# Performance work log

Measured on AMD Instinct MI355X. Metric: run time of the kernel, lower is better.

## Reference

```python
import jax, jax.numpy as jnp
import numpy as np

B, N, S, V, D, H, DEPTH, C = 4, 60000, 1024, 8, 256, 4, 4, 20
DH = D // H
MH = 4 * D
SCALE = 1.0 / float(np.sqrt(DH))


def _ln(x, g, b):
    m = x.mean(-1, keepdims=True)
    v = ((x - m) ** 2).mean(-1, keepdims=True)
    return g * (x - m) * jax.lax.rsqrt(v + 1e-5) + b


def _mha(q_in, kv_in, q_w, q_b, kv_w, kv_b, p_w, p_b):
    Bq, Tq, _ = q_in.shape
    Tk = kv_in.shape[1]
    q = (q_in @ q_w + q_b).reshape(Bq, Tq, H, DH)
    kv = (kv_in @ kv_w + kv_b).reshape(Bq, Tk, 2, H, DH)
    k, v = kv[:, :, 0], kv[:, :, 1]
    a = jax.nn.softmax(jnp.einsum('bqhd,bkhd->bhqk', q, k) * SCALE, axis=-1)
    o = jnp.einsum('bhqk,bkhd->bqhd', a, v).reshape(Bq, Tq, D)
    return o @ p_w + p_b, a


def _encoder(x, qkv_w, qkv_b, p_w, p_b, ln1_g, ln1_b, ln2_g, ln2_b, m_w1, m_b1, m_w2, m_b2):
    attns = []
    for d in range(DEPTH):
        h = _ln(x, ln1_g[d], ln1_b[d])
        o, a = _mha(h, h, qkv_w[d][:, :D], qkv_b[d][:D], qkv_w[d][:, D:], qkv_b[d][D:], p_w[d], p_b[d])
        x = x + o
        h = _ln(x, ln2_g[d], ln2_b[d])
        x = x + jax.nn.gelu(h @ m_w1[d] + m_b1[d]) @ m_w2[d] + m_b2[d]
        attns.append(a)
    return x, attns


def _seg_mean(x, ids):
    # scatter-mean (avg_grouping): x [N,F], ids [N] -> [S,F]; empty segments -> 0 (nan-fix in source)
    s = jax.ops.segment_sum(x, ids, num_segments=S)
    cnt = jax.ops.segment_sum(jnp.ones((x.shape[0],), x.dtype), ids, num_segments=S)
    return jnp.where(cnt[:, None] > 0, s / jnp.maximum(cnt, 1.0)[:, None], 0.0)


def _forward(supervoxel, point_feat, point_coord, image_view_tokens, cls_token, cls_pos_emb, view_pos_emb,
             pos_w1, pos_b1, pos_w2, pos_b2, pos_w3, pos_b3,
             enc_qkv_w, enc_qkv_b, enc_proj_w, enc_proj_b, enc_ln1_g, enc_ln1_b, enc_ln2_g, enc_ln2_b,
             enc_mlp_w1, enc_mlp_b1, enc_mlp_w2, enc_mlp_b2,
             dec_q_w, dec_q_b, dec_kv_w, dec_kv_b, dec_proj_w, dec_proj_b,
             dec_lnq_g, dec_lnq_b, dec_lnkv_g, dec_lnkv_b, dec_ln2_g, dec_ln2_b,
             dec_mlp_w1, dec_mlp_b1, dec_mlp_w2, dec_mlp_b2,
             head2d_w, head2d_b, head3d_w, head3d_b):
    # ---- view (2D) branch: [cls; view tokens] + pos, encoder idx 0 ----
    view_tok = jnp.concatenate([jnp.broadcast_to(cls_token, (B, C, D)), image_view_tokens], axis=1)
    view_pos = jnp.concatenate([jnp.broadcast_to(cls_pos_emb, (B, C, D)),
                                jnp.broadcast_to(view_pos_emb, (B, V, D))], axis=1)
    attn_view, _ = _encoder(view_tok + view_pos, enc_qkv_w[0], enc_qkv_b[0], enc_proj_w[0], enc_proj_b[0],
                            enc_ln1_g[0], enc_ln1_b[0], enc_ln2_g[0], enc_ln2_b[0],
                            enc_mlp_w1[0], enc_mlp_b1[0], enc_mlp_w2[0], enc_mlp_b2[0])
    mct_logits_2d = attn_view[:, :C].mean(-1)
    # ---- supervoxel scatter-mean pooling (the ragged core), vectorized over batch ----
    pooled_feat = jax.vmap(_seg_mean)(point_feat, supervoxel)      # [B,S,D]
    pooled_coord = jax.vmap(_seg_mean)(point_coord, supervoxel)    # [B,S,3]
    mean_target = jnp.take_along_axis(pooled_feat, supervoxel[..., None], axis=1)  # gather back [B,N,D]
    consistent_loss = jnp.mean((point_feat - mean_target) ** 2)
    # ---- coord positional MLP (3 layers) ----
    h = jax.nn.relu(pooled_coord @ pos_w1 + pos_b1)
    h = jax.nn.relu(h @ pos_w2 + pos_b2)
    pos = h @ pos_w3 + pos_b3
    # ---- voxel (3D) branch: [cls; pooled supervoxel tokens], encoder idx 1 ----
    vox_tok = jnp.concatenate([jnp.broadcast_to(cls_token, (B, C, D)), pooled_feat], axis=1)
    vox_pos = jnp.concatenate([jnp.broadcast_to(cls_pos_emb, (B, C, D)), pos], axis=1)
    vox_enc, _ = _encoder(vox_tok + vox_pos, enc_qkv_w[1], enc_qkv_b[1], enc_proj_w[1], enc_proj_b[1],
                          enc_ln1_g[1], enc_ln1_b[1], enc_ln2_g[1], enc_ln2_b[1],
                          enc_mlp_w1[1], enc_mlp_b1[1], enc_mlp_w2[1], enc_mlp_b2[1])
    mct_logits_3d = vox_enc[:, :C].mean(-1)
    # ---- interlance decoder: dual cross-attention, stream 0 = view->voxel, 1 = voxel->view ----
    view_x, vox_x = attn_view, vox_enc
    sim_losses = []
    for d in range(DEPTH):
        vq = _ln(view_x, dec_lnq_g[0, d], dec_lnq_b[0, d])
        xk = _ln(vox_x, dec_lnkv_g[0, d], dec_lnkv_b[0, d])
        xq = _ln(vox_x, dec_lnq_g[1, d], dec_lnq_b[1, d])
        vk = _ln(view_x, dec_lnkv_g[1, d], dec_lnkv_b[1, d])
        v_out, a = _mha(vq, xk, dec_q_w[0, d], dec_q_b[0, d], dec_kv_w[0, d], dec_kv_b[0, d], dec_proj_w[0, d], dec_proj_b[0, d])
        x_out, _ = _mha(xq, vk, dec_q_w[1, d], dec_q_b[1, d], dec_kv_w[1, d], dec_kv_b[1, d], dec_proj_w[1, d], dec_proj_b[1, d])
        view_x = view_x + v_out
        vox_x = vox_x + x_out
        hv = _ln(view_x, dec_ln2_g[0, d], dec_ln2_b[0, d])
        view_x = view_x + jax.nn.gelu(hv @ dec_mlp_w1[0, d] + dec_mlp_b1[0, d]) @ dec_mlp_w2[0, d] + dec_mlp_b2[0, d]
        hx = _ln(vox_x, dec_ln2_g[1, d], dec_ln2_b[1, d])
        vox_x = vox_x + jax.nn.gelu(hx @ dec_mlp_w1[1, d] + dec_mlp_b1[1, d]) @ dec_mlp_w2[1, d] + dec_mlp_b2[1, d]
        # pairwise token-sim loss on cls-cls block of head-averaged cross-attention
        sim = a.mean(1)[:, :C, :C]  # [B,C,C]
        lv = -jnp.diagonal(jax.nn.log_softmax(sim, axis=-1), axis1=1, axis2=2).mean(-1)
        lx = -jnp.diagonal(jax.nn.log_softmax(jnp.swapaxes(sim, 1, 2), axis=-1), axis1=1, axis2=2).mean(-1)
        sim_losses.append((lv + lx) * 0.5)
    token_sim_loss = jnp.stack(sim_losses).mean()
    cross_cls = (vox_x[:, :C] + view_x[:, :C]) * 0.5
    cross_mct_logits = cross_cls.mean(-1)
    # ---- CAM heads (cam_on_attn=True, pool='avg') ----
    voxel_cam = jax.nn.relu(vox_enc[:, C:]) @ head3d_w + head3d_b    # [B,S,C]
    view_cam = image_view_tokens @ head2d_w + head2d_b               # [B,V,C]
    cam_logits_3d = voxel_cam.mean(1)
    cam_logits_2d = view_cam.mean(1)
    return (cross_mct_logits, mct_logits_2d, mct_logits_3d, cam_logits_2d, cam_logits_3d,
            consistent_loss, token_sim_loss, voxel_cam)


def setup_inputs():
    key = jax.random.key(0)
    ks = iter(jax.random.split(key, 64))
    nrm = lambda *sh: jax.random.normal(next(ks), sh, jnp.float32)
    w = lambda *sh: 0.02 * jax.random.normal(next(ks), sh, jnp.float32)
    inp = dict(
        point_feat=nrm(B, N, D),
        point_coord=jax.random.uniform(next(ks), (B, N, 3), jnp.float32) * 100.0,
        image_view_tokens=nrm(B, V, D),
        supervoxel=jax.random.randint(next(ks), (B, N), 0, S),
        cls_token=w(1, C, D), cls_pos_emb=w(1, C, D), view_pos_emb=w(1, V, D),
        pos_w1=w(3, D), pos_b1=jnp.zeros((D,)), pos_w2=w(D, D), pos_b2=jnp.zeros((D,)),
        pos_w3=w(D, D), pos_b3=jnp.zeros((D,)),
        enc_qkv_w=w(2, DEPTH, D, 3 * D), enc_qkv_b=jnp.zeros((2, DEPTH, 3 * D)),
        enc_proj_w=w(2, DEPTH, D, D), enc_proj_b=jnp.zeros((2, DEPTH, D)),
        enc_ln1_g=jnp.ones((2, DEPTH, D)), enc_ln1_b=jnp.zeros((2, DEPTH, D)),
        enc_ln2_g=jnp.ones((2, DEPTH, D)), enc_ln2_b=jnp.zeros((2, DEPTH, D)),
        enc_mlp_w1=w(2, DEPTH, D, MH), enc_mlp_b1=jnp.zeros((2, DEPTH, MH)),
        enc_mlp_w2=w(2, DEPTH, MH, D), enc_mlp_b2=jnp.zeros((2, DEPTH, D)),
        dec_q_w=w(2, DEPTH, D, D), dec_q_b=jnp.zeros((2, DEPTH, D)),
        dec_kv_w=w(2, DEPTH, D, 2 * D), dec_kv_b=jnp.zeros((2, DEPTH, 2 * D)),
        dec_proj_w=w(2, DEPTH, D, D), dec_proj_b=jnp.zeros((2, DEPTH, D)),
        dec_lnq_g=jnp.ones((2, DEPTH, D)), dec_lnq_b=jnp.zeros((2, DEPTH, D)),
        dec_lnkv_g=jnp.ones((2, DEPTH, D)), dec_lnkv_b=jnp.zeros((2, DEPTH, D)),
        dec_ln2_g=jnp.ones((2, DEPTH, D)), dec_ln2_b=jnp.zeros((2, DEPTH, D)),
        dec_mlp_w1=w(2, DEPTH, D, MH), dec_mlp_b1=jnp.zeros((2, DEPTH, MH)),
        dec_mlp_w2=w(2, DEPTH, MH, D), dec_mlp_b2=jnp.zeros((2, DEPTH, D)),
        head2d_w=w(D, C), head2d_b=jnp.zeros((C,)),
        head3d_w=w(D, C), head3d_b=jnp.zeros((C,)),
    )
    return inp


def reference(point_feat, point_coord, image_view_tokens, supervoxel, cls_token, cls_pos_emb, view_pos_emb,
              pos_w1, pos_b1, pos_w2, pos_b2, pos_w3, pos_b3,
              enc_qkv_w, enc_qkv_b, enc_proj_w, enc_proj_b, enc_ln1_g, enc_ln1_b, enc_ln2_g, enc_ln2_b,
              enc_mlp_w1, enc_mlp_b1, enc_mlp_w2, enc_mlp_b2,
              dec_q_w, dec_q_b, dec_kv_w, dec_kv_b, dec_proj_w, dec_proj_b,
              dec_lnq_g, dec_lnq_b, dec_lnkv_g, dec_lnkv_b, dec_ln2_g, dec_ln2_b,
              dec_mlp_w1, dec_mlp_b1, dec_mlp_w2, dec_mlp_b2,
              head2d_w, head2d_b, head3d_w, head3d_b):
    return _forward(supervoxel, point_feat, point_coord, image_view_tokens, cls_token, cls_pos_emb, view_pos_emb,
                    pos_w1, pos_b1, pos_w2, pos_b2, pos_w3, pos_b3,
                    enc_qkv_w, enc_qkv_b, enc_proj_w, enc_proj_b, enc_ln1_g, enc_ln1_b, enc_ln2_g, enc_ln2_b,
                    enc_mlp_w1, enc_mlp_b1, enc_mlp_w2, enc_mlp_b2,
                    dec_q_w, dec_q_b, dec_kv_w, dec_kv_b, dec_proj_w, dec_proj_b,
                    dec_lnq_g, dec_lnq_b, dec_lnkv_g, dec_lnkv_b, dec_ln2_g, dec_ln2_b,
                    dec_mlp_w1, dec_mlp_b1, dec_mlp_w2, dec_mlp_b2,
                    head2d_w, head2d_b, head3d_w, head3d_b)
```

## Files before the change

### kernel.cpp

```cpp
#include <hip/hip_runtime.h>

namespace {

constexpr int kB = 4, kN = 60000, kS = 1024, kV = 8, kD = 256, kH = 4, kDepth = 4, kC = 20;
constexpr int kDH = 64;
constexpr int kMH = 1024;
constexpr int kTV = kC + kV;
constexpr int kTX = kC + kS;
constexpr float kScale = 0.125f;

constexpr int NSLICE = 8;
constexpr int DC = 16;
constexpr int DCH = kD / DC;

template <int BM, int BN, int TM, int TN, int ACT, bool TRB, bool PRELU>
__global__ __launch_bounds__(256) void gemm_k(
    const float* __restrict__ A, const float* __restrict__ Bm,
    const float* __restrict__ bias, const float* __restrict__ Res,
    float* __restrict__ C, int M, int N, int K, int lda, int ldb, int ldc,
    long sAb, long sAh, long sBb, long sBh, long sCb, long sCh, int Hdim, float alpha)
{
  constexpr int KT = 16;
  constexpr int MB = TM / 4;
  constexpr int NB = TN / 4;
  constexpr int AE = BM * KT / 256;
  constexpr int BE = BN * KT / 256;
  __shared__ float As[KT][BM + 4];
  __shared__ float Bs[KT][BN + 4];
  const int z = blockIdx.z;
  const int bi = z / Hdim, hi = z - bi * Hdim;
  A += (long)bi * sAb + (long)hi * sAh;
  Bm += (long)bi * sBb + (long)hi * sBh;
  C += (long)bi * sCb + (long)hi * sCh;
  const float* R = Res;
  if (R) R += (long)bi * sCb + (long)hi * sCh;
  const int n0 = blockIdx.x * BN, m0 = blockIdx.y * BM;
  const int tid = threadIdx.x;
  const int tx = tid % 16, ty = tid / 16;
  float acc[TM][TN];
#pragma unroll
  for (int i = 0; i < TM; i++)
#pragma unroll
    for (int j = 0; j < TN; j++) acc[i][j] = 0.f;

  float ra[AE], rb[BE];
#pragma unroll
  for (int i = 0; i < AE; i++) {
    int e = tid + i * 256;
    int row = e >> 4, kk = e & 15;
    int gm = m0 + row, gk = kk;
    float v = 0.f;
    if (gm < M && gk < K) v = A[(long)gm * lda + gk];
    if (PRELU) v = fmaxf(v, 0.f);
    ra[i] = v;
  }
#pragma unroll
  for (int i = 0; i < BE; i++) {
    int e = tid + i * 256;
    int kk, col;
    if (TRB) { kk = e & 15; col = e >> 4; }
    else     { col = e % BN; kk = e / BN; }
    int gk = kk, gn = n0 + col;
    float v = 0.f;
    if (gk < K && gn < N) v = TRB ? Bm[(long)gn * ldb + gk] : Bm[(long)gk * ldb + gn];
    rb[i] = v;
  }

  for (int k0 = 0; k0 < K; k0 += KT) {
#pragma unroll
    for (int i = 0; i < AE; i++) {
      int e = tid + i * 256;
      As[e & 15][e >> 4] = ra[i];
    }
#pragma unroll
    for (int i = 0; i < BE; i++) {
      int e = tid + i * 256;
      int kk, col;
      if (TRB) { kk = e & 15; col = e >> 4; }
      else     { col = e % BN; kk = e / BN; }
      Bs[kk][col] = rb[i];
    }
    __syncthreads();
    if (k0 + KT < K) {
      const int kn = k0 + KT;
#pragma unroll
      for (int i = 0; i < AE; i++) {
        int e = tid + i * 256;
        int row = e >> 4, kk = e & 15;
        int gm = m0 + row, gk = kn + kk;
        float v = 0.f;
        if (gm < M && gk < K) v = A[(long)gm * lda + gk];
        if (PRELU) v = fmaxf(v, 0.f);
        ra[i] = v;
      }
#pragma unroll
      for (int i = 0; i < BE; i++) {
        int e = tid + i * 256;
        int kk, col;
        if (TRB) { kk = e & 15; col = e >> 4; }
        else     { col = e % BN; kk = e / BN; }
        int gk = kn + kk, gn = n0 + col;
        float v = 0.f;
        if (gk < K && gn < N) v = TRB ? Bm[(long)gn * ldb + gk] : Bm[(long)gk * ldb + gn];
        rb[i] = v;
      }
    }
#pragma unroll
    for (int kk = 0; kk < KT; kk++) {
      const float4* Ar = reinterpret_cast<const float4*>(&As[kk][0]);
      const float4* Br = reinterpret_cast<const float4*>(&Bs[kk][0]);
      float4 af[MB], bf[NB];
#pragma unroll
      for (int ib = 0; ib < MB; ib++) af[ib] = Ar[ty + ib * 16];
#pragma unroll
      for (int jb = 0; jb < NB; jb++) bf[jb] = Br[tx + jb * 16];
      float av[TM], bv[TN];
#pragma unroll
      for (int ib = 0; ib < MB; ib++) {
        av[ib * 4 + 0] = af[ib].x; av[ib * 4 + 1] = af[ib].y;
        av[ib * 4 + 2] = af[ib].z; av[ib * 4 + 3] = af[ib].w;
      }
#pragma unroll
      for (int jb = 0; jb < NB; jb++) {
        bv[jb * 4 + 0] = bf[jb].x; bv[jb * 4 + 1] = bf[jb].y;
        bv[jb * 4 + 2] = bf[jb].z; bv[jb * 4 + 3] = bf[jb].w;
      }
#pragma unroll
      for (int i = 0; i < TM; i++)
#pragma unroll
        for (int j = 0; j < TN; j++) acc[i][j] += av[i] * bv[j];
    }
    __syncthreads();
  }
#pragma unroll
  for (int i = 0; i < TM; i++) {
    int gm = m0 + (i >> 2) * 64 + ty * 4 + (i & 3);
    if (gm >= M) continue;
#pragma unroll
    for (int j = 0; j < TN; j++) {
      int gn = n0 + (j >> 2) * 64 + tx * 4 + (j & 3);
      if (gn >= N) continue;
      float v = acc[i][j] * alpha;
      if (bias) v += bias[gn];
      if (ACT == 1) v = fmaxf(v, 0.f);
      else if (ACT == 2) {
        float u = v;
        float t = 0.7978845608028654f * (u + 0.044715f * u * u * u);
        v = u / (1.f + __expf(-2.f * t));
      }
      if (R) v += R[(long)gm * ldc + gn];
      C[(long)gm * ldc + gn] = v;
    }
  }
}

__global__ __launch_bounds__(256) void ln_k(const float* __restrict__ x,
                                            const float* __restrict__ g,
                                            const float* __restrict__ b,
                                            float* __restrict__ o, int rows)
{
  __shared__ float red[256];
  __shared__ float stat;
  int row = blockIdx.x;
  int t = threadIdx.x;
  float v = x[(long)row * kD + t];
  red[t] = v;
  __syncthreads();
  for (int s = 128; s > 0; s >>= 1) { if (t < s) red[t] += red[t + s]; __syncthreads(); }
  if (t == 0) stat = red[0] * (1.f / kD);
  __syncthreads();
  float m = stat;
  float d = v - m;
  red[t] = d * d;
  __syncthreads();
  for (int s = 128; s > 0; s >>= 1) { if (t < s) red[t] += red[t + s]; __syncthreads(); }
  if (t == 0) stat = rsqrtf(red[0] * (1.f / kD) + 1e-5f);
  __syncthreads();
  o[(long)row * kD + t] = g[t] * d * stat + b[t];
}

__global__ __launch_bounds__(256) void softmax_k(float* __restrict__ s, int L)
{
  long row = blockIdx.x;
  float* p = s + row * (long)L;
  int t = threadIdx.x;
  float rv[8];
  int nc = (L + 255) >> 8;
  float mx = -1e30f;
  for (int c = 0; c < nc; c++) {
    int i = t + c * 256;
    rv[c] = (i < L) ? p[i] : -1e30f;
    mx = fmaxf(mx, rv[c]);
  }
  __shared__ float red[256];
  __shared__ float bb;
  red[t] = mx; __syncthreads();
  for (int st = 128; st > 0; st >>= 1) { if (t < st) red[t] = fmaxf(red[t], red[t + st]); __syncthreads(); }
  if (t == 0) bb = red[0];
  __syncthreads();
  float bm = bb;
  float sum = 0.f;
  for (int c = 0; c < nc; c++) {
    int i = t + c * 256;
    if (i < L) { rv[c] = __expf(rv[c] - bm); sum += rv[c]; }
  }
  red[t] = sum; __syncthreads();
  for (int st = 128; st > 0; st >>= 1) { if (t < st) red[t] += red[t + st]; __syncthreads(); }
  if (t == 0) bb = 1.f / red[0];
  __syncthreads();
  float inv = bb;
  for (int c = 0; c < nc; c++) {
    int i = t + c * 256;
    if (i < L) p[i] = rv[c] * inv;
  }
}

__global__ __launch_bounds__(256) void segsum_k(const float* __restrict__ pf,
                                                const int* __restrict__ sv,
                                                float* __restrict__ part)
{
  __shared__ float acc[kS * DC];
  int t = threadIdx.x;
  for (int i = t; i < kS * DC; i += 256) acc[i] = 0.f;
  __syncthreads();
  int dc = blockIdx.x, sl = blockIdx.y, b = blockIdx.z;
  const int per = kN / NSLICE;
  int n0 = sl * per, n1 = n0 + per;
  int ld_ = t & (DC - 1), pg = t >> 4;
  for (int base = n0 + pg; base < n1; base += 16 * 8) {
    int s[8]; float v[8];
#pragma unroll
    for (int u = 0; u < 8; u++) {
      int n = base + u * 16;
      bool ok = n < n1;
      s[u] = ok ? sv[b * kN + n] : -1;
      v[u] = ok ? pf[((long)b * kN + n) * kD + dc * DC + ld_] : 0.f;
    }
#pragma unroll
    for (int u = 0; u < 8; u++)
      if (s[u] >= 0) atomicAdd(&acc[s[u] * DC + ld_], v[u]);
  }
  __syncthreads();
  float* outp = part + (((long)(b * NSLICE + sl) * DCH + dc) * (kS * DC));
  for (int i = t; i < kS * DC; i += 256) outp[i] = acc[i];
}

__global__ __launch_bounds__(256) void segmeta_k(const float* __restrict__ pc,
                                                 const int* __restrict__ sv,
                                                 float* __restrict__ cpart,
                                                 float* __restrict__ csumpart)
{
  __shared__ float meta[kS * 4];
  int t = threadIdx.x;
  for (int i = t; i < kS * 4; i += 256) meta[i] = 0.f;
  __syncthreads();
  int sl = blockIdx.x, b = blockIdx.y;
  const int per = kN / NSLICE;
  int n0 = sl * per, n1 = n0 + per;
  for (int base = n0 + t; base < n1; base += 256 * 4) {
    int s[4]; float cx[4], cy[4], cz[4];
#pragma unroll
    for (int u = 0; u < 4; u++) {
      int n = base + u * 256;
      bool ok = n < n1;
      s[u] = ok ? sv[b * kN + n] : -1;
      long p = ((long)b * kN + n) * 3;
      cx[u] = ok ? pc[p + 0] : 0.f;
      cy[u] = ok ? pc[p + 1] : 0.f;
      cz[u] = ok ? pc[p + 2] : 0.f;
    }
#pragma unroll
    for (int u = 0; u < 4; u++)
      if (s[u] >= 0) {
        atomicAdd(&meta[s[u] * 4 + 0], 1.f);
        atomicAdd(&meta[s[u] * 4 + 1], cx[u]);
        atomicAdd(&meta[s[u] * 4 + 2], cy[u]);
        atomicAdd(&meta[s[u] * 4 + 3], cz[u]);
      }
  }
  __syncthreads();
  float* oc = cpart + (long)(b * NSLICE + sl) * kS;
  for (int i = t; i < kS; i += 256) oc[i] = meta[i * 4];
  float* os = csumpart + (long)(b * NSLICE + sl) * kS * 3;
  for (int i = t; i < kS * 3; i += 256) {
    int s2 = i / 3, j = i - s2 * 3;
    os[i] = meta[s2 * 4 + 1 + j];
  }
}

__global__ void cntfin_k(const float* __restrict__ cpart, float* __restrict__ counts)
{
  int i = blockIdx.x * 256 + threadIdx.x;
  if (i >= kB * kS) return;
  int b = i / kS, s = i - b * kS;
  float c = 0.f;
  for (int sl = 0; sl < NSLICE; sl++) c += cpart[(long)(b * NSLICE + sl) * kS + s];
  counts[i] = c;
}

__global__ void poolfin_k(const float* __restrict__ part, const float* __restrict__ counts,
                          float* __restrict__ pooled)
{
  long i = (long)blockIdx.x * 256 + threadIdx.x;
  if (i >= (long)kB * kS * kD) return;
  int d = (int)(i % kD);
  long bs = i / kD;
  int s = (int)(bs % kS), b = (int)(bs / kS);
  int dc = d / DC, dl = d - dc * DC;
  float sum = 0.f;
  for (int sl = 0; sl < NSLICE; sl++)
    sum += part[(((long)(b * NSLICE + sl) * DCH + dc) * (kS * DC)) + s * DC + dl];
  float c = counts[b * kS + s];
  pooled[i] = (c > 0.5f) ? sum / c : 0.f;
}

__global__ void coordfin_k(const float* __restrict__ csumpart, const float* __restrict__ counts,
                           float* __restrict__ pcoord)
{
  int i = blockIdx.x * 256 + threadIdx.x;
  if (i >= kB * kS * 3) return;
  int bs = i / 3, j = i - bs * 3;
  int b = bs / kS, s = bs - b * kS;
  float sum = 0.f;
  for (int sl = 0; sl < NSLICE; sl++)
    sum += csumpart[((long)(b * NSLICE + sl) * kS + s) * 3 + j];
  float c = counts[bs];
  pcoord[i] = (c > 0.5f) ? sum / c : 0.f;
}

__global__ __launch_bounds__(256) void closs_k(const float* __restrict__ pf,
                                               const int* __restrict__ sv,
                                               const float* __restrict__ pooled,
                                               float* __restrict__ outp)
{
  const long total = (long)kB * kN * (kD / 4);
  float a = 0.f;
  for (long i = (long)blockIdx.x * 256 + threadIdx.x; i < total; i += (long)gridDim.x * 256) {
    long pnt = i >> 6;
    int dc = (int)(i & 63);
    int b = (int)(pnt / kN);
    int s = sv[pnt];
    float4 v = ((const float4*)pf)[i];
    float4 m = ((const float4*)pooled)[((long)b * kS + s) * (kD / 4) + dc];
    float dx = v.x - m.x, dy = v.y - m.y, dz = v.z - m.z, dw = v.w - m.w;
    a += dx * dx + dy * dy + dz * dz + dw * dw;
  }
  __shared__ float red[256];
  red[threadIdx.x] = a; __syncthreads();
  for (int s = 128; s > 0; s >>= 1) { if (threadIdx.x < s) red[threadIdx.x] += red[threadIdx.x + s]; __syncthreads(); }
  if (threadIdx.x == 0) atomicAdd(outp, red[0]);
}

__global__ void build_k(const float* __restrict__ cls, const float* __restrict__ clspos,
                        const float* __restrict__ tok, const float* __restrict__ pos,
                        float* __restrict__ x, int T, int Tt, int posBatched)
{
  long i = (long)blockIdx.x * 256 + threadIdx.x;
  long tot = (long)kB * T * kD;
  if (i >= tot) return;
  int d = (int)(i % kD);
  long bt = i / kD;
  int t = (int)(bt % T), b = (int)(bt / T);
  float v;
  if (t < kC) v = cls[t * kD + d] + clspos[t * kD + d];
  else {
    int tt = t - kC;
    v = tok[((long)b * Tt + tt) * kD + d] +
        pos[((long)(posBatched ? b * Tt : 0) + tt) * kD + d];
  }
  x[i] = v;
}

__global__ __launch_bounds__(64) void simloss_k(const float* __restrict__ probs,
                                                float* __restrict__ accum)
{
  int b = blockIdx.x;
  __shared__ float sim[kC][kC];
  int t = threadIdx.x;
  for (int e = t; e < kC * kC; e += 64) {
    int i = e / kC, j = e - i * kC;
    float s = 0.f;
    for (int h = 0; h < kH; h++)
      s += probs[(((long)(b * kH + h)) * kTV + i) * kTX + j];
    sim[i][j] = s * (1.f / kH);
  }
  __syncthreads();
  float local = 0.f;
  if (t < kC) {
    int i = t;
    float mx = -1e30f;
    for (int j = 0; j < kC; j++) mx = fmaxf(mx, sim[i][j]);
    float se = 0.f;
    for (int j = 0; j < kC; j++) se += expf(sim[i][j] - mx);
    float dr = sim[i][i] - mx - logf(se);
    float mc = -1e30f;
    for (int j = 0; j < kC; j++) mc = fmaxf(mc, sim[j][i]);
    float sc = 0.f;
    for (int j = 0; j < kC; j++) sc += expf(sim[j][i] - mc);
    float dcl = sim[i][i] - mc - logf(sc);
    local = dr + dcl;
  }
  for (int o = 32; o > 0; o >>= 1) local += __shfl_down(local, o);
  if (t == 0) atomicAdd(accum, local * (-0.5f / kC));
}

__global__ __launch_bounds__(64) void meanD_k(const float* __restrict__ x,
                                              float* __restrict__ o, int T)
{
  int bc = blockIdx.x;
  int b = bc / kC, c = bc - b * kC;
  const float* r = x + ((long)b * T + c) * kD;
  float s = 0.f;
  for (int d = threadIdx.x; d < kD; d += 64) s += r[d];
  for (int w = 32; w > 0; w >>= 1) s += __shfl_down(s, w);
  if (threadIdx.x == 0) o[bc] = s * (1.f / kD);
}

__global__ __launch_bounds__(64) void cross_k(const float* __restrict__ xv,
                                              const float* __restrict__ xw,
                                              float* __restrict__ o)
{
  int bc = blockIdx.x;
  int b = bc / kC, c = bc - b * kC;
  const float* rv = xv + ((long)b * kTX + c) * kD;
  const float* rw = xw + ((long)b * kTV + c) * kD;
  float s = 0.f;
  for (int d = threadIdx.x; d < kD; d += 64) s += 0.5f * (rv[d] + rw[d]);
  for (int w = 32; w > 0; w >>= 1) s += __shfl_down(s, w);
  if (threadIdx.x == 0) o[bc] = s * (1.f / kD);
}

__global__ __launch_bounds__(256) void cam3d_k(const float* __restrict__ vc,
                                               float* __restrict__ o)
{
  __shared__ float red[256];
  int bc = blockIdx.x;
  int b = bc / kC, c = bc - b * kC;
  float s = 0.f;
  for (int t = threadIdx.x; t < kS; t += 256) s += vc[((long)b * kS + t) * kC + c];
  red[threadIdx.x] = s; __syncthreads();
  for (int st = 128; st > 0; st >>= 1) { if (threadIdx.x < st) red[threadIdx.x] += red[threadIdx.x + st]; __syncthreads(); }
  if (threadIdx.x == 0) o[bc] = red[0] * (1.f / kS);
}

__global__ void meanv_k(const float* __restrict__ ivt, float* __restrict__ mv)
{
  int i = blockIdx.x * 256 + threadIdx.x;
  if (i >= kB * kD) return;
  int b = i / kD, d = i - b * kD;
  float s = 0.f;
  for (int v = 0; v < kV; v++) s += ivt[((long)b * kV + v) * kD + d];
  mv[i] = s * (1.f / kV);
}

__global__ __launch_bounds__(64) void cam2d_k(const float* __restrict__ mv,
                                              const float* __restrict__ w2,
                                              const float* __restrict__ b2,
                                              float* __restrict__ o)
{
  int bc = blockIdx.x;
  int b = bc / kC, c = bc - b * kC;
  float s = 0.f;
  for (int d = threadIdx.x; d < kD; d += 64) s += mv[b * kD + d] * w2[d * kC + c];
  for (int w = 32; w > 0; w >>= 1) s += __shfl_down(s, w);
  if (threadIdx.x == 0) o[bc] = s + b2[c];
}

__global__ void fin_k(const float* __restrict__ cl, const float* __restrict__ ts,
                      float* __restrict__ outp)
{
  outp[400] = cl[0] * (1.f / ((float)kB * (float)kN * (float)kD));
  outp[401] = ts[0] * (1.f / (kDepth * kB));
}

static void gemm_disp(hipStream_t st, const float* A, const float* Bm, const float* bias,
                      const float* Res, float* C, int M, int N, int K,
                      int lda, int ldb, int ldc,
                      long sAb, long sAh, long sBb, long sBh, long sCb, long sCh,
                      int Z, int Hdim, float alpha, int act, bool trb, bool prelu)
{
  dim3 blk(256, 1, 1);
  long bigBlocks = (long)((M + 127) / 128) * ((N + 127) / 128) * Z;
  bool big = (N >= 96) && (bigBlocks >= 384);
#define GARGS A, Bm, bias, Res, C, M, N, K, lda, ldb, ldc, sAb, sAh, sBb, sBh, sCb, sCh, Hdim, alpha
  if (big) {
    dim3 g((N + 127) / 128, (M + 127) / 128, Z);
    if (prelu)          gemm_k<128, 128, 8, 8, 0, false, true ><<<g, blk, 0, st>>>(GARGS);
    else if (trb)       gemm_k<128, 128, 8, 8, 0, true,  false><<<g, blk, 0, st>>>(GARGS);
    else if (act == 1)  gemm_k<128, 128, 8, 8, 1, false, false><<<g, blk, 0, st>>>(GARGS);
    else if (act == 2)  gemm_k<128, 128, 8, 8, 2, false, false><<<g, blk, 0, st>>>(GARGS);
    else                gemm_k<128, 128, 8, 8, 0, false, false><<<g, blk, 0, st>>>(GARGS);
  } else {
    dim3 g((N + 63) / 64, (M + 63) / 64, Z);
    if (prelu)          gemm_k<64, 64, 4, 4, 0, false, true ><<<g, blk, 0, st>>>(GARGS);
    else if (trb)       gemm_k<64, 64, 4, 4, 0, true,  false><<<g, blk, 0, st>>>(GARGS);
    else if (act == 1)  gemm_k<64, 64, 4, 4, 1, false, false><<<g, blk, 0, st>>>(GARGS);
    else if (act == 2)  gemm_k<64, 64, 4, 4, 2, false, false><<<g, blk, 0, st>>>(GARGS);
    else                gemm_k<64, 64, 4, 4, 0, false, false><<<g, blk, 0, st>>>(GARGS);
  }
#undef GARGS
}

static void linear(hipStream_t st, const float* A, const float* W, const float* bias,
                   const float* Res, float* C, int M, int N, int K, int act)
{
  gemm_disp(st, A, W, bias, Res, C, M, N, K, K, N, N, 0, 0, 0, 0, 0, 0, 1, 1, 1.f, act, false, false);
}

static void attention(hipStream_t st, const float* qb, int ldq, const float* kb,
                      const float* vb, int ldkv, int Tq, int Tk, float* P, float* O)
{
  gemm_disp(st, qb, kb, nullptr, nullptr, P, Tq, Tk, kDH, ldq, ldkv, Tk,
            (long)Tq * ldq, kDH, (long)Tk * ldkv, kDH, (long)kH * Tq * Tk, (long)Tq * Tk,
            kB * kH, kH, kScale, 0, true, false);
  softmax_k<<<dim3(kB * kH * Tq), dim3(256), 0, st>>>(P, Tk);
  gemm_disp(st, P, vb, nullptr, nullptr, O, Tq, kDH, Tk, Tk, ldkv, kD,
            (long)kH * Tq * Tk, (long)Tq * Tk, (long)Tk * ldkv, kDH, (long)Tq * kD, kDH,
            kB * kH, kH, 1.f, 0, false, false);
}

}

extern "C" void kernel_launch(void* const* d_in, const int* in_sizes, int n_in,
                              void* d_out, int out_size, void* d_ws, size_t ws_size,
                              hipStream_t stream)
{
  (void)in_sizes; (void)n_in; (void)out_size; (void)ws_size;
  const float* point_feat  = (const float*)d_in[0];
  const float* point_coord = (const float*)d_in[1];
  const float* ivt         = (const float*)d_in[2];
  const int*   sv          = (const int*)d_in[3];
  const float* cls_token   = (const float*)d_in[4];
  const float* cls_pos     = (const float*)d_in[5];
  const float* view_pos    = (const float*)d_in[6];
  const float* pos_w1 = (const float*)d_in[7];
  const float* pos_b1 = (const float*)d_in[8];
  const float* pos_w2 = (const float*)d_in[9];
  const float* pos_b2 = (const float*)d_in[10];
  const float* pos_w3 = (const float*)d_in[11];
  const float* pos_b3 = (const float*)d_in[12];
  const float* enc_qkv_w  = (const float*)d_in[13];
  const float* enc_qkv_b  = (const float*)d_in[14];
  const float* enc_proj_w = (const float*)d_in[15];
  const float* enc_proj_b = (const float*)d_in[16];
  const float* enc_ln1_g  = (const float*)d_in[17];
  const float* enc_ln1_b  = (const float*)d_in[18];
  const float* enc_ln2_g  = (const float*)d_in[19];
  const float* enc_ln2_b  = (const float*)d_in[20];
  const float* enc_mlp_w1 = (const float*)d_in[21];
  const float* enc_mlp_b1 = (const float*)d_in[22];
  const float* enc_mlp_w2 = (const float*)d_in[23];
  const float* enc_mlp_b2 = (const float*)d_in[24];
  const float* dec_q_w    = (const float*)d_in[25];
  const float* dec_q_b    = (const float*)d_in[26];
  const float* dec_kv_w   = (const float*)d_in[27];
  const float* dec_kv_b   = (const float*)d_in[28];
  const float* dec_proj_w = (const float*)d_in[29];
  const float* dec_proj_b = (const float*)d_in[30];
  const float* dec_lnq_g  = (const float*)d_in[31];
  const float* dec_lnq_b  = (const float*)d_in[32];
  const float* dec_lnkv_g = (const float*)d_in[33];
  const float* dec_lnkv_b = (const float*)d_in[34];
  const float* dec_ln2_g  = (const float*)d_in[35];
  const float* dec_ln2_b  = (const float*)d_in[36];
  const float* dec_mlp_w1 = (const float*)d_in[37];
  const float* dec_mlp_b1 = (const float*)d_in[38];
  const float* dec_mlp_w2 = (const float*)d_in[39];
  const float* dec_mlp_b2 = (const float*)d_in[40];
  const float* head2d_w = (const float*)d_in[41];
  const float* head2d_b = (const float*)d_in[42];
  const float* head3d_w = (const float*)d_in[43];
  const float* head3d_b = (const float*)d_in[44];
  float* out = (float*)d_out;

  float* w = (float*)d_ws;
  size_t off = 0;
  auto alloc = [&](size_t n) { float* p = w + off; off += n; return p; };

  const size_t scores_sz = (size_t)kB * kH * kTX * kTX;
  const size_t probs_sz  = (size_t)kB * kH * kTV * kTX;
  float* regionA  = alloc(scores_sz + 2 * probs_sz);
  float* seg_part = regionA;
  float* scores   = regionA;
  float* probs1   = regionA + scores_sz;
  float* probs2   = probs1 + probs_sz;

  float* cpart    = alloc((size_t)kB * NSLICE * kS);
  float* csumpart = alloc((size_t)kB * NSLICE * kS * 3);
  float* counts   = alloc((size_t)kB * kS);
  float* pooled   = alloc((size_t)kB * kS * kD);
  float* closs    = alloc(1);
  float* simacc   = alloc(1);
  float* pcoord   = alloc((size_t)kB * kS * 3);
  float* ph1      = alloc((size_t)kB * kS * kD);
  float* ph2      = alloc((size_t)kB * kS * kD);
  float* posb     = alloc((size_t)kB * kS * kD);
  float* x_view   = alloc((size_t)kB * kTV * kD);
  float* h_view   = alloc((size_t)kB * kTV * kD);
  float* qkv_view = alloc((size_t)kB * kTV * 3 * kD);
  float* o_view   = alloc((size_t)kB * kTV * kD);
  float* mlp_view = alloc((size_t)kB * kTV * kMH);
  float* x_vox    = alloc((size_t)kB * kTX * kD);
  float* h_vox    = alloc((size_t)kB * kTX * kD);
  float* qkv_vox  = alloc((size_t)kB * kTX * 3 * kD);
  float* o_vox    = alloc((size_t)kB * kTX * kD);
  float* mlp_vox  = alloc((size_t)kB * kTX * kMH);
  float* q_small  = alloc((size_t)kB * kTV * kD);
  float* kv_big   = alloc((size_t)kB * kTX * 2 * kD);
  float* q_big    = alloc((size_t)kB * kTX * kD);
  float* kv_small = alloc((size_t)kB * kTV * 2 * kD);
  float* meanv    = alloc((size_t)kB * kD);

  hipMemsetAsync(closs, 0, 2 * sizeof(float), stream);

  segsum_k<<<dim3(DCH, NSLICE, kB), 256, 0, stream>>>(point_feat, sv, seg_part);
  segmeta_k<<<dim3(NSLICE, kB), 256, 0, stream>>>(point_coord, sv, cpart, csumpart);
  cntfin_k<<<dim3((kB * kS + 255) / 256), 256, 0, stream>>>(cpart, counts);
  poolfin_k<<<dim3((kB * kS * kD + 255) / 256), 256, 0, stream>>>(seg_part, counts, pooled);
  coordfin_k<<<dim3((kB * kS * 3 + 255) / 256), 256, 0, stream>>>(csumpart, counts, pcoord);
  closs_k<<<dim3(2048), 256, 0, stream>>>(point_feat, sv, pooled, closs);

  linear(stream, pcoord, pos_w1, pos_b1, nullptr, ph1, kB * kS, kD, 3, 1);
  linear(stream, ph1, pos_w2, pos_b2, nullptr, ph2, kB * kS, kD, kD, 1);
  linear(stream, ph2, pos_w3, pos_b3, nullptr, posb, kB * kS, kD, kD, 0);

  build_k<<<dim3(((unsigned)(kB * kTV * kD) + 255) / 256), 256, 0, stream>>>(
      cls_token, cls_pos, ivt, view_pos, x_view, kTV, kV, 0);
  build_k<<<dim3(((unsigned)(kB * kTX * kD) + 255) / 256), 256, 0, stream>>>(
      cls_token, cls_pos, pooled, posb, x_vox, kTX, kS, 1);

  auto encoder = [&](float* x, int T, int e, float* h, float* qkv, float* o, float* mlp) {
    int M = kB * T;
    for (int dl = 0; dl < kDepth; dl++) {
      int wi = e * kDepth + dl;
      ln_k<<<dim3(M), 256, 0, stream>>>(x, enc_ln1_g + wi * kD, enc_ln1_b + wi * kD, h, M);
      linear(stream, h, enc_qkv_w + (long)wi * kD * 3 * kD, enc_qkv_b + (long)wi * 3 * kD,
             nullptr, qkv, M, 3 * kD, kD, 0);
      attention(stream, qkv, 3 * kD, qkv + kD, qkv + 2 * kD, 3 * kD, T, T, scores, o);
      linear(stream, o, enc_proj_w + (long)wi * kD * kD, enc_proj_b + (long)wi * kD, x, x, M, kD, kD, 0);
      ln_k<<<dim3(M), 256, 0, stream>>>(x, enc_ln2_g + wi * kD, enc_ln2_b + wi * kD, h, M);
      linear(stream, h, enc_mlp_w1 + (long)wi * kD * kMH, enc_mlp_b1 + (long)wi * kMH,
             nullptr, mlp, M, kMH, kD, 2);
      linear(stream, mlp, enc_mlp_w2 + (long)wi * kMH * kD, enc_mlp_b2 + (long)wi * kD, x, x, M, kD, kMH, 0);
    }
  };
  encoder(x_view, kTV, 0, h_view, qkv_view, o_view, mlp_view);
  meanD_k<<<dim3(kB * kC), 64, 0, stream>>>(x_view, out + 80, kTV);

  encoder(x_vox, kTX, 1, h_vox, qkv_vox, o_vox, mlp_vox);
  meanD_k<<<dim3(kB * kC), 64, 0, stream>>>(x_vox, out + 160, kTX);

  gemm_disp(stream, x_vox + (long)kC * kD, head3d_w, head3d_b, nullptr, out + 402,
            kS, kC, kD, kD, kC, kC,
            (long)kTX * kD, 0, 0, 0, (long)kS * kC, 0,
            kB, 1, 1.f, 0, false, true);
  cam3d_k<<<dim3(kB * kC), 256, 0, stream>>>(out + 402, out + 320);
  meanv_k<<<dim3((kB * kD + 255) / 256), 256, 0, stream>>>(ivt, meanv);
  cam2d_k<<<dim3(kB * kC), 64, 0, stream>>>(meanv, head2d_w, head2d_b, out + 240);

  for (int dl = 0; dl < kDepth; dl++) {
    int w0 = dl, w1 = kDepth + dl;
    ln_k<<<dim3(kB * kTV), 256, 0, stream>>>(x_view, dec_lnq_g + w0 * kD, dec_lnq_b + w0 * kD, h_view, kB * kTV);
    ln_k<<<dim3(kB * kTX), 256, 0, stream>>>(x_vox, dec_lnkv_g + w0 * kD, dec_lnkv_b + w0 * kD, h_vox, kB * kTX);
    linear(stream, h_view, dec_q_w + (long)w0 * kD * kD, dec_q_b + (long)w0 * kD, nullptr, q_small, kB * kTV, kD, kD, 0);
    linear(stream, h_vox, dec_kv_w + (long)w0 * kD * 2 * kD, dec_kv_b + (long)w0 * 2 * kD, nullptr, kv_big, kB * kTX, 2 * kD, kD, 0);
    attention(stream, q_small, kD, kv_big, kv_big + kD, 2 * kD, kTV, kTX, probs1, o_view);
    simloss_k<<<dim3(kB), 64, 0, stream>>>(probs1, simacc);

    ln_k<<<dim3(kB * kTX), 256, 0, stream>>>(x_vox, dec_lnq_g + w1 * kD, dec_lnq_b + w1 * kD, h_vox, kB * kTX);
    ln_k<<<dim3(kB * kTV), 256, 0, stream>>>(x_view, dec_lnkv_g + w1 * kD, dec_lnkv_b + w1 * kD, h_view, kB * kTV);
    linear(stream, h_vox, dec_q_w + (long)w1 * kD * kD, dec_q_b + (long)w1 * kD, nullptr, q_big, kB * kTX, kD, kD, 0);
    linear(stream, h_view, dec_kv_w + (long)w1 * kD * 2 * kD, dec_kv_b + (long)w1 * 2 * kD, nullptr, kv_small, kB * kTV, 2 * kD, kD, 0);
    attention(stream, q_big, kD, kv_small, kv_small + kD, 2 * kD, kTX, kTV, probs2, o_vox);

    linear(stream, o_view, dec_proj_w + (long)w0 * kD * kD, dec_proj_b + (long)w0 * kD, x_view, x_view, kB * kTV, kD, kD, 0);
    linear(stream, o_vox, dec_proj_w + (long)w1 * kD * kD, dec_proj_b + (long)w1 * kD, x_vox, x_vox, kB * kTX, kD, kD, 0);

    ln_k<<<dim3(kB * kTV), 256, 0, stream>>>(x_view, dec_ln2_g + w0 * kD, dec_ln2_b + w0 * kD, h_view, kB * kTV);
    linear(stream, h_view, dec_mlp_w1 + (long)w0 * kD * kMH, dec_mlp_b1 + (long)w0 * kMH, nullptr, mlp_view, kB * kTV, kMH, kD, 2);
    linear(stream, mlp_view, dec_mlp_w2 + (long)w0 * kMH * kD, dec_mlp_b2 + (long)w0 * kD, x_view, x_view, kB * kTV, kD, kMH, 0);
    ln_k<<<dim3(kB * kTX), 256, 0, stream>>>(x_vox, dec_ln2_g + w1 * kD, dec_ln2_b + w1 * kD, h_vox, kB * kTX);
    linear(stream, h_vox, dec_mlp_w1 + (long)w1 * kD * kMH, dec_mlp_b1 + (long)w1 * kMH, nullptr, mlp_vox, kB * kTX, kMH, kD, 2);
    linear(stream, mlp_vox, dec_mlp_w2 + (long)w1 * kMH * kD, dec_mlp_b2 + (long)w1 * kD, x_vox, x_vox, kB * kTX, kD, kMH, 0);
  }

  cross_k<<<dim3(kB * kC), 64, 0, stream>>>(x_vox, x_view, out + 0);
  fin_k<<<dim3(1), 1, 0, stream>>>(closs, simacc, out);
}
```

Before: 5.315 ms.

## Add split-bf16 MFMA GEMM for large voxel-branch matmuls and attention

Adds a matrix-core GEMM kernel that splits each fp32 operand into high and low bf16 parts and accumulates three MFMA products, approximating fp32 accuracy. It uses a swizzled LDS layout and register prefetch of the next K tile. The kernel replaces the scalar fp32 GEMM for the voxel encoder, decoder voxel-side linears and voxel attention. It also retunes the segment-sum kernel to 512 threads with a smaller unroll. The split adds conversion work and carries a small precision risk versus true fp32.

```diff
diff --git a/kernel.cpp b/kernel.cpp
--- a/kernel.cpp
+++ b/kernel.cpp
@@ -12,6 +12,184 @@
 constexpr int NSLICE = 8;
 constexpr int DC = 16;
 constexpr int DCH = kD / DC;
+
+typedef short bf16x8 __attribute__((ext_vector_type(8)));
+typedef float f32x4 __attribute__((ext_vector_type(4)));
+typedef int   int4v __attribute__((ext_vector_type(4)));
+
+__device__ inline short f2bf_rne(float f) {
+  unsigned u = __builtin_bit_cast(unsigned, f);
+  u += 0x7FFF + ((u >> 16) & 1);
+  return (short)(u >> 16);
+}
+__device__ inline float bf2f(short s) {
+  unsigned u = ((unsigned)(unsigned short)s) << 16;
+  return __builtin_bit_cast(float, u);
+}
+__device__ inline void split8(const float* v, int4v& hi, int4v& lo) {
+  short h[8], l[8];
+#pragma unroll
+  for (int j = 0; j < 8; j++) {
+    h[j] = f2bf_rne(v[j]);
+    l[j] = f2bf_rne(v[j] - bf2f(h[j]));
+  }
+#pragma unroll
+  for (int j = 0; j < 4; j++) {
+    hi[j] = (int)(unsigned short)h[2*j] | ((int)(unsigned short)h[2*j+1] << 16);
+    lo[j] = (int)(unsigned short)l[2*j] | ((int)(unsigned short)l[2*j+1] << 16);
+  }
+}
+
+template <int ACT, bool TRB>
+__global__ __launch_bounds__(256) void mgemm_k(
+    const float* __restrict__ A, const float* __restrict__ Bm,
+    const float* __restrict__ bias, const float* __restrict__ Res,
+    float* __restrict__ C, int M, int N, int K, int lda, int ldb, int ldc,
+    long sAb, long sAh, long sBb, long sBh, long sCb, long sCh, int Hdim, float alpha)
+{
+  __shared__ char lds[2 * 128 * 128];
+  char* Alds = lds;
+  char* Blds = lds + 128 * 128;
+  const int z = blockIdx.z;
+  const int bi = z / Hdim, hi_ = z - bi * Hdim;
+  A += (long)bi * sAb + (long)hi_ * sAh;
+  Bm += (long)bi * sBb + (long)hi_ * sBh;
+  C += (long)bi * sCb + (long)hi_ * sCh;
+  const float* R = Res;
+  if (R) R += (long)bi * sCb + (long)hi_ * sCh;
+  const int n0 = blockIdx.x * 128, m0 = blockIdx.y * 128;
+  const int tid = threadIdx.x;
+  const int lane = tid & 63, wid = tid >> 6;
+  const int wm = wid >> 1, wn = wid & 1;
+
+  f32x4 acc[4][4];
+#pragma unroll
+  for (int i = 0; i < 4; i++)
+#pragma unroll
+    for (int j = 0; j < 4; j++) { acc[i][j][0]=0.f; acc[i][j][1]=0.f; acc[i][j][2]=0.f; acc[i][j][3]=0.f; }
+
+  int4v paH[2], paL[2], pbH[2], pbL[2];
+
+  auto loadA = [&](int k0) {
+#pragma unroll
+    for (int i = 0; i < 2; i++) {
+      int c = tid + i * 256;
+      int row = c >> 2, kg = c & 3;
+      int gm = m0 + row;
+      int gk0 = k0 + kg * 8;
+      float v[8];
+      if (gm < M && gk0 + 8 <= K) {
+        float4 x = *(const float4*)(A + (long)gm * lda + gk0);
+        float4 y = *(const float4*)(A + (long)gm * lda + gk0 + 4);
+        v[0]=x.x; v[1]=x.y; v[2]=x.z; v[3]=x.w; v[4]=y.x; v[5]=y.y; v[6]=y.z; v[7]=y.w;
+      } else {
+#pragma unroll
+        for (int j = 0; j < 8; j++)
+          v[j] = (gm < M && gk0 + j < K) ? A[(long)gm * lda + gk0 + j] : 0.f;
+      }
+      split8(v, paH[i], paL[i]);
+    }
+  };
+  auto loadB = [&](int k0) {
+#pragma unroll
+    for (int i = 0; i < 2; i++) {
+      int c = tid + i * 256;
+      float v[8];
+      if (TRB) {
+        int row = c >> 2, kg = c & 3;
+        int gn = n0 + row, gk0 = k0 + kg * 8;
+        if (gn < N && gk0 + 8 <= K) {
+          float4 x = *(const float4*)(Bm + (long)gn * ldb + gk0);
+          float4 y = *(const float4*)(Bm + (long)gn * ldb + gk0 + 4);
+          v[0]=x.x; v[1]=x.y; v[2]=x.z; v[3]=x.w; v[4]=y.x; v[5]=y.y; v[6]=y.z; v[7]=y.w;
+        } else {
+#pragma unroll
+          for (int j = 0; j < 8; j++)
+            v[j] = (gn < N && gk0 + j < K) ? Bm[(long)gn * ldb + gk0 + j] : 0.f;
+        }
+      } else {
+        int n = c & 127, kg = c >> 7;
+        int gn = n0 + n, gk0 = k0 + kg * 8;
+#pragma unroll
+        for (int j = 0; j < 8; j++)
+          v[j] = (gn < N && gk0 + j < K) ? Bm[(long)(gk0 + j) * ldb + gn] : 0.f;
+      }
+      split8(v, pbH[i], pbL[i]);
+    }
+  };
+  auto commit = [&]() {
+#pragma unroll
+    for (int i = 0; i < 2; i++) {
+      int c = tid + i * 256;
+      {
+        int row = c >> 2, kg = c & 3;
+        *(int4v*)(Alds + row * 128 + (((kg    ) ^ (row & 7)) << 4)) = paH[i];
+        *(int4v*)(Alds + row * 128 + (((kg + 4) ^ (row & 7)) << 4)) = paL[i];
+      }
+      {
+        int row, kg;
+        if (TRB) { row = c >> 2; kg = c & 3; }
+        else     { row = c & 127; kg = c >> 7; }
+        *(int4v*)(Blds + row * 128 + (((kg    ) ^ (row & 7)) << 4)) = pbH[i];
+        *(int4v*)(Blds + row * 128 + (((kg + 4) ^ (row & 7)) << 4)) = pbL[i];
+      }
+    }
+  };
+
+  loadA(0); loadB(0);
+
+  const int r16 = lane & 15, kg0 = lane >> 4;
+  for (int k0 = 0; k0 < K; k0 += 32) {
+    commit();
+    __syncthreads();
+    if (k0 + 32 < K) { loadA(k0 + 32); loadB(k0 + 32); }
+    bf16x8 aH[4], aL[4];
+#pragma unroll
+    for (int mt = 0; mt < 4; mt++) {
+      int row = wm * 64 + mt * 16 + r16;
+      aH[mt] = *(const bf16x8*)(Alds + row * 128 + (((kg0    ) ^ (row & 7)) << 4));
+      aL[mt] = *(const bf16x8*)(Alds + row * 128 + (((kg0 + 4) ^ (row & 7)) << 4));
+    }
+#pragma unroll
+    for (int nt = 0; nt < 4; nt++) {
+      int col = wn * 64 + nt * 16 + r16;
+      bf16x8 bH = *(const bf16x8*)(Blds + col * 128 + (((kg0    ) ^ (col & 7)) << 4));
+      bf16x8 bL = *(const bf16x8*)(Blds + col * 128 + (((kg0 + 4) ^ (col & 7)) << 4));
+#pragma unroll
+      for (int mt = 0; mt < 4; mt++) {
+        acc[mt][nt] = __builtin_amdgcn_mfma_f32_16x16x32_bf16(aH[mt], bH, acc[mt][nt], 0, 0, 0);
+        acc[mt][nt] = __builtin_amdgcn_mfma_f32_16x16x32_bf16(aH[mt], bL, acc[mt][nt], 0, 0, 0);
+        acc[mt][nt] = __builtin_amdgcn_mfma_f32_16x16x32_bf16(aL[mt], bH, acc[mt][nt], 0, 0, 0);
+      }
+    }
+    __syncthreads();
+  }
+
+  const int rg = lane >> 4;
+#pragma unroll
+  for (int mt = 0; mt < 4; mt++) {
+#pragma unroll
+    for (int nt = 0; nt < 4; nt++) {
+      int gn = n0 + wn * 64 + nt * 16 + r16;
+      if (gn >= N) continue;
+#pragma unroll
+      for (int r = 0; r < 4; r++) {
+        int gm = m0 + wm * 64 + mt * 16 + rg * 4 + r;
+        if (gm >= M) continue;
+        float v = acc[mt][nt][r] * alpha;
+        if (bias) v += bias[gn];
+        if (ACT == 1) v = fmaxf(v, 0.f);
+        else if (ACT == 2) {
+          float u = v;
+          float t = 0.7978845608028654f * (u + 0.044715f * u * u * u);
+          v = u / (1.f + __expf(-2.f * t));
+        }
+        if (R) v += R[(long)gm * ldc + gn];
+        C[(long)gm * ldc + gn] = v;
+      }
+    }
+  }
+}
 
 template <int BM, int BN, int TM, int TN, int ACT, bool TRB, bool PRELU>
 __global__ __launch_bounds__(256) void gemm_k(
@@ -215,34 +393,34 @@
   }
 }
 
-__global__ __launch_bounds__(256) void segsum_k(const float* __restrict__ pf,
+__global__ __launch_bounds__(512) void segsum_k(const float* __restrict__ pf,
                                                 const int* __restrict__ sv,
                                                 float* __restrict__ part)
 {
   __shared__ float acc[kS * DC];
   int t = threadIdx.x;
-  for (int i = t; i < kS * DC; i += 256) acc[i] = 0.f;
+  for (int i = t; i < kS * DC; i += 512) acc[i] = 0.f;
   __syncthreads();
   int dc = blockIdx.x, sl = blockIdx.y, b = blockIdx.z;
   const int per = kN / NSLICE;
   int n0 = sl * per, n1 = n0 + per;
   int ld_ = t & (DC - 1), pg = t >> 4;
-  for (int base = n0 + pg; base < n1; base += 16 * 8) {
-    int s[8]; float v[8];
-#pragma unroll
-    for (int u = 0; u < 8; u++) {
-      int n = base + u * 16;
+  for (int base = n0 + pg; base < n1; base += 32 * 4) {
+    int s[4]; float v[4];
+#pragma unroll
+    for (int u = 0; u < 4; u++) {
+      int n = base + u * 32;
       bool ok = n < n1;
       s[u] = ok ? sv[b * kN + n] : -1;
       v[u] = ok ? pf[((long)b * kN + n) * kD + dc * DC + ld_] : 0.f;
     }
 #pragma unroll
-    for (int u = 0; u < 8; u++)
+    for (int u = 0; u < 4; u++)
       if (s[u] >= 0) atomicAdd(&acc[s[u] * DC + ld_], v[u]);
   }
   __syncthreads();
   float* outp = part + (((long)(b * NSLICE + sl) * DCH + dc) * (kS * DC));
-  for (int i = t; i < kS * DC; i += 256) outp[i] = acc[i];
+  for (int i = t; i < kS * DC; i += 512) outp[i] = acc[i];
 }
 
 __global__ __launch_bounds__(256) void segmeta_k(const float* __restrict__ pc,
@@ -501,10 +679,31 @@
 #undef GARGS
 }
 
+static void mgemm_disp(hipStream_t st, const float* A, const float* Bm, const float* bias,
+                       const float* Res, float* C, int M, int N, int K,
+                       int lda, int ldb, int ldc,
+                       long sAb, long sAh, long sBb, long sBh, long sCb, long sCh,
+                       int Z, int Hdim, float alpha, int act, bool trb)
+{
+  dim3 blk(256, 1, 1);
+  dim3 g((N + 127) / 128, (M + 127) / 128, Z);
+#define GARGS A, Bm, bias, Res, C, M, N, K, lda, ldb, ldc, sAb, sAh, sBb, sBh, sCb, sCh, Hdim, alpha
+  if (trb)            mgemm_k<0, true ><<<g, blk, 0, st>>>(GARGS);
+  else if (act == 2)  mgemm_k<2, false><<<g, blk, 0, st>>>(GARGS);
+  else                mgemm_k<0, false><<<g, blk, 0, st>>>(GARGS);
+#undef GARGS
+}
+
 static void linear(hipStream_t st, const float* A, const float* W, const float* bias,
                    const float* Res, float* C, int M, int N, int K, int act)
 {
   gemm_disp(st, A, W, bias, Res, C, M, N, K, K, N, N, 0, 0, 0, 0, 0, 0, 1, 1, 1.f, act, false, false);
+}
+
+static void linear_mf(hipStream_t st, const float* A, const float* W, const float* bias,
+                      const float* Res, float* C, int M, int N, int K, int act)
+{
+  mgemm_disp(st, A, W, bias, Res, C, M, N, K, K, N, N, 0, 0, 0, 0, 0, 0, 1, 1, 1.f, act, false);
 }
 
 static void attention(hipStream_t st, const float* qb, int ldq, const float* kb,
@@ -517,6 +716,18 @@
   gemm_disp(st, P, vb, nullptr, nullptr, O, Tq, kDH, Tk, Tk, ldkv, kD,
             (long)kH * Tq * Tk, (long)Tq * Tk, (long)Tk * ldkv, kDH, (long)Tq * kD, kDH,
             kB * kH, kH, 1.f, 0, false, false);
+}
+
+static void attention_mf(hipStream_t st, const float* qb, int ldq, const float* kb,
+                         const float* vb, int ldkv, int Tq, int Tk, float* P, float* O)
+{
+  mgemm_disp(st, qb, kb, nullptr, nullptr, P, Tq, Tk, kDH, ldq, ldkv, Tk,
+             (long)Tq * ldq, kDH, (long)Tk * ldkv, kDH, (long)kH * Tq * Tk, (long)Tq * Tk,
+             kB * kH, kH, kScale, 0, true);
+  softmax_k<<<dim3(kB * kH * Tq), dim3(256), 0, st>>>(P, Tk);
+  mgemm_disp(st, P, vb, nullptr, nullptr, O, Tq, kDH, Tk, Tk, ldkv, kD,
+             (long)kH * Tq * Tk, (long)Tq * Tk, (long)Tk * ldkv, kDH, (long)Tq * kD, kDH,
+             kB * kH, kH, 1.f, 0, false);
 }
 
 }
@@ -613,7 +824,7 @@
 
   hipMemsetAsync(closs, 0, 2 * sizeof(float), stream);
 
-  segsum_k<<<dim3(DCH, NSLICE, kB), 256, 0, stream>>>(point_feat, sv, seg_part);
+  segsum_k<<<dim3(DCH, NSLICE, kB), 512, 0, stream>>>(point_feat, sv, seg_part);
   segmeta_k<<<dim3(NSLICE, kB), 256, 0, stream>>>(point_coord, sv, cpart, csumpart);
   cntfin_k<<<dim3((kB * kS + 255) / 256), 256, 0, stream>>>(cpart, counts);
   poolfin_k<<<dim3((kB * kS * kD + 255) / 256), 256, 0, stream>>>(seg_part, counts, pooled);
@@ -629,25 +840,36 @@
   build_k<<<dim3(((unsigned)(kB * kTX * kD) + 255) / 256), 256, 0, stream>>>(
       cls_token, cls_pos, pooled, posb, x_vox, kTX, kS, 1);
 
-  auto encoder = [&](float* x, int T, int e, float* h, float* qkv, float* o, float* mlp) {
+  auto encoder = [&](float* x, int T, int e, float* h, float* qkv, float* o, float* mlp, bool mf) {
     int M = kB * T;
     for (int dl = 0; dl < kDepth; dl++) {
       int wi = e * kDepth + dl;
       ln_k<<<dim3(M), 256, 0, stream>>>(x, enc_ln1_g + wi * kD, enc_ln1_b + wi * kD, h, M);
-      linear(stream, h, enc_qkv_w + (long)wi * kD * 3 * kD, enc_qkv_b + (long)wi * 3 * kD,
-             nullptr, qkv, M, 3 * kD, kD, 0);
-      attention(stream, qkv, 3 * kD, qkv + kD, qkv + 2 * kD, 3 * kD, T, T, scores, o);
-      linear(stream, o, enc_proj_w + (long)wi * kD * kD, enc_proj_b + (long)wi * kD, x, x, M, kD, kD, 0);
-      ln_k<<<dim3(M), 256, 0, stream>>>(x, enc_ln2_g + wi * kD, enc_ln2_b + wi * kD, h, M);
-      linear(stream, h, enc_mlp_w1 + (long)wi * kD * kMH, enc_mlp_b1 + (long)wi * kMH,
-             nullptr, mlp, M, kMH, kD, 2);
-      linear(stream, mlp, enc_mlp_w2 + (long)wi * kMH * kD, enc_mlp_b2 + (long)wi * kD, x, x, M, kD, kMH, 0);
+      if (mf) {
+        linear_mf(stream, h, enc_qkv_w + (long)wi * kD * 3 * kD, enc_qkv_b + (long)wi * 3 * kD,
+                  nullptr, qkv, M, 3 * kD, kD, 0);
+        attention_mf(stream, qkv, 3 * kD, qkv + kD, qkv + 2 * kD, 3 * kD, T, T, scores, o);
+        linear_mf(stream, o, enc_proj_w + (long)wi * kD * kD, enc_proj_b + (long)wi * kD, x, x, M, kD, kD, 0);
+        ln_k<<<dim3(M), 256, 0, stream>>>(x, enc_ln2_g + wi * kD, enc_ln2_b + wi * kD, h, M);
+        linear_mf(stream, h, enc_mlp_w1 + (long)wi * kD * kMH, enc_mlp_b1 + (long)wi * kMH,
+                  nullptr, mlp, M, kMH, kD, 2);
+        linear_mf(stream, mlp, enc_mlp_w2 + (long)wi * kMH * kD, enc_mlp_b2 + (long)wi * kD, x, x, M, kD, kMH, 0);
+      } else {
+        linear(stream, h, enc_qkv_w + (long)wi * kD * 3 * kD, enc_qkv_b + (long)wi * 3 * kD,
+               nullptr, qkv, M, 3 * kD, kD, 0);
+        attention(stream, qkv, 3 * kD, qkv + kD, qkv + 2 * kD, 3 * kD, T, T, scores, o);
+        linear(stream, o, enc_proj_w + (long)wi * kD * kD, enc_proj_b + (long)wi * kD, x, x, M, kD, kD, 0);
+        ln_k<<<dim3(M), 256, 0, stream>>>(x, enc_ln2_g + wi * kD, enc_ln2_b + wi * kD, h, M);
+        linear(stream, h, enc_mlp_w1 + (long)wi * kD * kMH, enc_mlp_b1 + (long)wi * kMH,
+               nullptr, mlp, M, kMH, kD, 2);
+        linear(stream, mlp, enc_mlp_w2 + (long)wi * kMH * kD, enc_mlp_b2 + (long)wi * kD, x, x, M, kD, kMH, 0);
+      }
     }
   };
-  encoder(x_view, kTV, 0, h_view, qkv_view, o_view, mlp_view);
+  encoder(x_view, kTV, 0, h_view, qkv_view, o_view, mlp_view, false);
   meanD_k<<<dim3(kB * kC), 64, 0, stream>>>(x_view, out + 80, kTV);
 
-  encoder(x_vox, kTX, 1, h_vox, qkv_vox, o_vox, mlp_vox);
+  encoder(x_vox, kTX, 1, h_vox, qkv_vox, o_vox, mlp_vox, true);
   meanD_k<<<dim3(kB * kC), 64, 0, stream>>>(x_vox, out + 160, kTX);
 
   gemm_disp(stream, x_vox + (long)kC * kD, head3d_w, head3d_b, nullptr, out + 402,
@@ -663,25 +885,25 @@
     ln_k<<<dim3(kB * kTV), 256, 0, stream>>>(x_view, dec_lnq_g + w0 * kD, dec_lnq_b + w0 * kD, h_view, kB * kTV);
     ln_k<<<dim3(kB * kTX), 256, 0, stream>>>(x_vox, dec_lnkv_g + w0 * kD, dec_lnkv_b + w0 * kD, h_vox, kB * kTX);
     linear(stream, h_view, dec_q_w + (long)w0 * kD * kD, dec_q_b + (long)w0 * kD, nullptr, q_small, kB * kTV, kD, kD, 0);
-    linear(stream, h_vox, dec_kv_w + (long)w0 * kD * 2 * kD, dec_kv_b + (long)w0 * 2 * kD, nullptr, kv_big, kB * kTX, 2 * kD, kD, 0);
+    linear_mf(stream, h_vox, dec_kv_w + (long)w0 * kD * 2 * kD, dec_kv_b + (long)w0 * 2 * kD, nullptr, kv_big, kB * kTX, 2 * kD, kD, 0);
     attention(stream, q_small, kD, kv_big, kv_big + kD, 2 * kD, kTV, kTX, probs1, o_view);
     simloss_k<<<dim3(kB), 64, 0, stream>>>(probs1, simacc);
 
     ln_k<<<dim3(kB * kTX), 256, 0, stream>>>(x_vox, dec_lnq_g + w1 * kD, dec_lnq_b + w1 * kD, h_vox, kB * kTX);
     ln_k<<<dim3(kB * kTV), 256, 0, stream>>>(x_view, dec_lnkv_g + w1 * kD, dec_lnkv_b + w1 * kD, h_view, kB * kTV);
-    linear(stream, h_vox, dec_q_w + (long)w1 * kD * kD, dec_q_b + (long)w1 * kD, nullptr, q_big, kB * kTX, kD, kD, 0);
+    linear_mf(stream, h_vox, dec_q_w + (long)w1 * kD * kD, dec_q_b + (long)w1 * kD, nullptr, q_big, kB * kTX, kD, kD, 0);
     linear(stream, h_view, dec_kv_w + (long)w1 * kD * 2 * kD, dec_kv_b + (long)w1 * 2 * kD, nullptr, kv_small, kB * kTV, 2 * kD, kD, 0);
-    attention(stream, q_big, kD, kv_small, kv_small + kD, 2 * kD, kTX, kTV, probs2, o_vox);
+    attention_mf(stream, q_big, kD, kv_small, kv_small + kD, 2 * kD, kTX, kTV, probs2, o_vox);
 
     linear(stream, o_view, dec_proj_w + (long)w0 * kD * kD, dec_proj_b + (long)w0 * kD, x_view, x_view, kB * kTV, kD, kD, 0);
-    linear(stream, o_vox, dec_proj_w + (long)w1 * kD * kD, dec_proj_b + (long)w1 * kD, x_vox, x_vox, kB * kTX, kD, kD, 0);
+    linear_mf(stream, o_vox, dec_proj_w + (long)w1 * kD * kD, dec_proj_b + (long)w1 * kD, x_vox, x_vox, kB * kTX, kD, kD, 0);
 
     ln_k<<<dim3(kB * kTV), 256, 0, stream>>>(x_view, dec_ln2_g + w0 * kD, dec_ln2_b + w0 * kD, h_view, kB * kTV);
     linear(stream, h_view, dec_mlp_w1 + (long)w0 * kD * kMH, dec_mlp_b1 + (long)w0 * kMH, nullptr, mlp_view, kB * kTV, kMH, kD, 2);
     linear(stream, mlp_view, dec_mlp_w2 + (long)w0 * kMH * kD, dec_mlp_b2 + (long)w0 * kD, x_view, x_view, kB * kTV, kD, kMH, 0);
     ln_k<<<dim3(kB * kTX), 256, 0, stream>>>(x_vox, dec_ln2_g + w1 * kD, dec_ln2_b + w1 * kD, h_vox, kB * kTX);
-    linear(stream, h_vox, dec_mlp_w1 + (long)w1 * kD * kMH, dec_mlp_b1 + (long)w1 * kMH, nullptr, mlp_vox, kB * kTX, kMH, kD, 2);
-    linear(stream, mlp_vox, dec_mlp_w2 + (long)w1 * kMH * kD, dec_mlp_b2 + (long)w1 * kD, x_vox, x_vox, kB * kTX, kD, kMH, 0);
+    linear_mf(stream, h_vox, dec_mlp_w1 + (long)w1 * kD * kMH, dec_mlp_b1 + (long)w1 * kMH, nullptr, mlp_vox, kB * kTX, kMH, kD, 2);
+    linear_mf(stream, mlp_vox, dec_mlp_w2 + (long)w1 * kMH * kD, dec_mlp_b2 + (long)w1 * kD, x_vox, x_vox, kB * kTX, kD, kMH, 0);
   }
 
   cross_k<<<dim3(kB * kC), 64, 0, stream>>>(x_vox, x_view, out + 0);
```

After: 5.589 ms. 1.05x slower.
